# Performance work log

Measured on AMD Instinct MI355X. Metric: run time of the kernel, lower is better.

## Reference

```python
import jax, jax.numpy as jnp
import numpy as np

H = 4
HD = 32
C = 128
NU = 40000
NI = 40000
E = 200000


def _linear(x, W, b):
    # torch Linear: y = x @ W.T + b, W is [out, in]
    return x @ W.T + b


def _counts_in(query, sorted_keys):
    l = jnp.searchsorted(sorted_keys, query, side='left')
    r = jnp.searchsorted(sorted_keys, query, side='right')
    return (r - l).astype(jnp.float32)


def _segment_softmax(scores, seg, n):
    # scores: [E, H], seg: [E] destination ids
    m = jax.ops.segment_max(scores, seg, num_segments=n)
    m = jnp.where(jnp.isfinite(m), m, 0.0)
    e = jnp.exp(scores - m[seg])
    z = jax.ops.segment_sum(e, seg, num_segments=n)
    return e / z[seg]


def _deg_count(idx, n):
    return jnp.zeros((n,), jnp.float32).at[idx].add(1.0)


def _layernorm(x):
    mu = x.mean(-1, keepdims=True)
    var = ((x - mu) ** 2).mean(-1, keepdims=True)
    return (x - mu) / jnp.sqrt(var + 1e-5)


def _relation(x_src, x_dst, src, dst, t_src, t_dst,
              Wq, bq, Wk, bk, Wv, bv, Wo, bo,
              head_bias, beta, tau_raw, gamma, delta,
              counts, recips, n_dst):
    Q = _linear(x_dst, Wq, bq).reshape(-1, H, HD)
    K = _linear(x_src, Wk, bk).reshape(-1, H, HD)
    V = _linear(x_src, Wv, bv).reshape(-1, H, HD)
    Qe, Ke, Ve = Q[dst], K[src], V[src]                      # [E, H, HD]
    scores = (Qe * Ke).sum(-1) / jnp.sqrt(jnp.float32(HD))   # [E, H]
    scores = scores + head_bias
    dt = jnp.abs(t_dst[dst] - t_src[src]) + 1e-6
    tau = jax.nn.softplus(tau_raw) + 1e-6
    scores = scores + (-jnp.log1p(dt / tau))[:, None] * beta
    scores = scores + jnp.log1p(counts)[:, None] * gamma
    scores = scores + recips[:, None] * delta
    w = _segment_softmax(scores, dst, n_dst)                 # [E, H]
    out_e = (Ve * w[:, :, None]).reshape(-1, C)
    out_e = _linear(out_e, Wo, bo)
    return jnp.zeros((n_dst, C), x_dst.dtype).at[dst].add(out_e)


def setup_inputs() -> dict:
    key = jax.random.key(0)
    ks = jax.random.split(key, 20)
    inp = {
        'x_user': jax.random.normal(ks[0], (NU, C), jnp.float32),
        'x_item': jax.random.normal(ks[1], (NI, C), jnp.float32),
        't_user': jax.random.uniform(ks[2], (NU,), jnp.float32) * 100.0,
        't_item': jax.random.uniform(ks[3], (NI,), jnp.float32) * 100.0,
        'edge_index_ui': jax.random.randint(ks[4], (2, E), 0, NU, jnp.int32),
        'edge_index_iu': jax.random.randint(ks[5], (2, E), 0, NI, jnp.int32),
        'Wq': jax.random.normal(ks[6], (C, C), jnp.float32) * 0.05,
        'bq': jax.random.normal(ks[7], (C,), jnp.float32) * 0.05,
        'Wk': jax.random.normal(ks[8], (C, C), jnp.float32) * 0.05,
        'bk': jax.random.normal(ks[9], (C,), jnp.float32) * 0.05,
        'Wv': jax.random.normal(ks[10], (C, C), jnp.float32) * 0.05,
        'bv': jax.random.normal(ks[11], (C,), jnp.float32) * 0.05,
        'Wo': jax.random.normal(ks[12], (C, C), jnp.float32) * 0.05,
        'bo': jax.random.normal(ks[13], (C,), jnp.float32) * 0.05,
        'rel_head_bias': jax.random.normal(ks[14], (2, H), jnp.float32) * 0.1,
        'time_beta': jax.random.normal(ks[15], (2, H), jnp.float32) * 0.1,
        'time_tau_raw': jax.random.normal(ks[16], (2,), jnp.float32),
        'gamma_multirel': jax.random.normal(ks[17], (2, H), jnp.float32) * 0.1,
        'delta_recip': jax.random.normal(ks[18], (2, H), jnp.float32) * 0.1,
    }
    return inp


def reference(x_user, x_item, t_user, t_item, edge_index_ui, edge_index_iu,
              Wq, bq, Wk, bk, Wv, bv, Wo, bo,
              rel_head_bias, time_beta, time_tau_raw, gamma_multirel, delta_recip):
    su, du = edge_index_ui[0], edge_index_ui[1]   # user -> item
    si, di = edge_index_iu[0], edge_index_iu[1]   # item -> user
    # multirel counts (pair multiplicity - 1) and reciprocity flags, per relation
    pid_ui = su * NI + du            # (user,item) pair ids (fits int32: NU*NI < 2^31)
    pid_iu = si * NU + di            # (item,user) pair ids
    rev_for_ui = di * NI + si        # reversed pairs of iu edges in (user,item) space
    rev_for_iu = du * NU + su        # reversed pairs of ui edges in (item,user) space
    counts_ui = _counts_in(pid_ui, jnp.sort(pid_ui)) - 1.0
    counts_iu = _counts_in(pid_iu, jnp.sort(pid_iu)) - 1.0
    recips_ui = (_counts_in(pid_ui, jnp.sort(rev_for_ui)) > 0).astype(jnp.float32)
    recips_iu = (_counts_in(pid_iu, jnp.sort(rev_for_iu)) > 0).astype(jnp.float32)

    out_item = _relation(x_user, x_item, su, du, t_user, t_item,
                         Wq, bq, Wk, bk, Wv, bv, Wo, bo,
                         rel_head_bias[0], time_beta[0], time_tau_raw[0],
                         gamma_multirel[0], delta_recip[0], counts_ui, recips_ui, NI)
    out_user = _relation(x_item, x_user, si, di, t_item, t_user,
                         Wq, bq, Wk, bk, Wv, bv, Wo, bo,
                         rel_head_bias[1], time_beta[1], time_tau_raw[1],
                         gamma_multirel[1], delta_recip[1], counts_iu, recips_iu, NU)
    # degree centrality bias: total (in + out) degree added to every channel
    deg_user = _deg_count(su, NU) + _deg_count(di, NU)
    deg_item = _deg_count(du, NI) + _deg_count(si, NI)
    out_user = out_user + deg_user[:, None]
    out_item = out_item + deg_item[:, None]
    return _layernorm(out_user + x_user), _layernorm(out_item + x_item)
```

## Files before the change

kernel.cpp:

```cpp
#include <hip/hip_runtime.h>
#include <math.h>

constexpr int kH  = 4;
constexpr int kHD = 32;
constexpr int kC  = 128;
constexpr int kNU = 40000;
constexpr int kNI = 40000;
constexpr int kE  = 200000;
constexpr int kNT = kNU + kNI;
constexpr int kTS = 1 << 19;
constexpr int kTMASK = kTS - 1;
constexpr int kSB = (kNT + 1023) / 1024;
constexpr int kTilesPerSide = kNU / 16;
constexpr int kTiles = kNT / 16;
constexpr int kGemmBlocks  = 768;
constexpr int kTableBlocks = 1536;
constexpr int kFusedBlocks = 2304;

#define DEV_INLINE __device__ __forceinline__

typedef short bf16x8 __attribute__((ext_vector_type(8)));
typedef float f32x4  __attribute__((ext_vector_type(4)));
typedef uint32_t u32x4 __attribute__((ext_vector_type(4)));
typedef unsigned long long u64;

DEV_INLINE int hash_slot(int pid) {
  uint32_t h = (uint32_t)pid * 2654435761u;
  return (int)((h >> 13) & kTMASK);
}

DEV_INLINE unsigned short f2bf(float f) {
  uint32_t u = __float_as_uint(f);
  u += 0x7fffu + ((u >> 16) & 1u);
  return (unsigned short)(u >> 16);
}

DEV_INLINE float bflo(uint32_t u) { return __uint_as_float(u << 16); }
DEV_INLINE float bfhi(uint32_t u) { return __uint_as_float(u & 0xffff0000u); }

DEV_INLINE int swz(int row, int elem) {
  return (elem & 7) | (((elem >> 3) ^ (row & 7)) << 3);
}

constexpr u64 kEmpty64 = ~0ULL;

DEV_INLINE void table_insert64(u64* __restrict__ keys, int pid) {
  int slot = hash_slot(pid);
  const u64 want = (u64)(uint32_t)pid | (1ULL << 32);
  for (;;) {
    u64 old = atomicCAS(&keys[slot], kEmpty64, want);
    if (old == kEmpty64) return;
    if ((uint32_t)old == (uint32_t)pid) {
      atomicAdd(&keys[slot], 1ULL << 32);
      return;
    }
    slot = (slot + 1) & kTMASK;
  }
}

DEV_INLINE int table_count64(const u64* __restrict__ keys, int pid) {
  int slot = hash_slot(pid);
  for (;;) {
    u64 k = keys[slot];
    if ((uint32_t)k == (uint32_t)pid) return (int)(k >> 32);
    if (k == kEmpty64) return 0;
    slot = (slot + 1) & kTMASK;
  }
}

__global__ void cast4w_bf16(const float* __restrict__ w0, const float* __restrict__ w1,
                            const float* __restrict__ w2, const float* __restrict__ w3,
                            unsigned short* __restrict__ o0, unsigned short* __restrict__ o1,
                            unsigned short* __restrict__ o2, unsigned short* __restrict__ o3) {
  int i = blockIdx.x * blockDim.x + threadIdx.x;
  int m = i >> 12, j = i & 4095;
  const float* in = (m == 0) ? w0 : (m == 1) ? w1 : (m == 2) ? w2 : w3;
  unsigned short* out = (m == 0) ? o0 : (m == 1) ? o1 : (m == 2) ? o2 : o3;
  float4 v = ((const float4*)in)[j];
  ushort4 o = {f2bf(v.x), f2bf(v.y), f2bf(v.z), f2bf(v.w)};
  ((ushort4*)out)[j] = o;
}

__global__ __launch_bounds__(256, 3) void qkv_build(
    const float* __restrict__ Xu, const float* __restrict__ Xi,
    const unsigned short* __restrict__ Wq, const unsigned short* __restrict__ Wk,
    const unsigned short* __restrict__ Wv,
    const float* __restrict__ bq, const float* __restrict__ bk,
    const float* __restrict__ bv,
    unsigned short* __restrict__ Qu, unsigned short* __restrict__ Ku,
    unsigned short* __restrict__ Vu,
    unsigned short* __restrict__ Qi, unsigned short* __restrict__ Ki,
    unsigned short* __restrict__ Vi,
    const int* __restrict__ su, const int* __restrict__ du,
    const int* __restrict__ si, const int* __restrict__ di,
    u64* __restrict__ keyA, u64* __restrict__ keyB,
    int* __restrict__ deg_all, int* __restrict__ pos_all) {
  __shared__ unsigned short sx[16 * kC];
  __shared__ unsigned short sr[3 * 16 * kC];
  const int bid = blockIdx.x;
  const int tid = threadIdx.x;

  if (bid % 3 != 1) {
    const int tb = (bid / 3) * 2 + ((bid % 3) ? 1 : 0);
    for (int t = tb * 256 + tid; t < 2 * kE; t += kTableBlocks * 256) {
      if (t < kE) {
        int s = su[t], d = du[t];
        table_insert64(keyA, s * kNI + d);
        pos_all[t] = atomicAdd(&deg_all[d], 1);
      } else {
        int e = t - kE;
        int s = si[e], d = di[e];
        table_insert64(keyB, s * kNU + d);
        pos_all[t] = atomicAdd(&deg_all[kNI + d], 1);
      }
    }
    return;
  }

  const int gb   = bid / 3;
  const int wave = tid >> 6;
  const int lane = tid & 63;
  const int mr   = lane & 15;
  const int quad = lane >> 4;
  const int ct0  = wave * 2;
  const int srow = tid >> 4;
  const int schk = tid & 15;

  bf16x8 wf[3][2][4];
  {
    const unsigned short* Ws[3] = {Wq, Wk, Wv};
#pragma unroll
    for (int m = 0; m < 3; ++m)
#pragma unroll
      for (int c = 0; c < 2; ++c) {
        const unsigned short* wrow = Ws[m] + (size_t)((ct0 + c) * 16 + mr) * kC + quad * 8;
#pragma unroll
        for (int kc = 0; kc < 4; ++kc) wf[m][c][kc] = *(const bf16x8*)(wrow + kc * 32);
      }
  }

  int tile = gb;
  float4 xa, xb;
  {
    const bool item = tile >= kTilesPerSide;
    const float* X = item ? Xi : Xu;
    const int base = (item ? tile - kTilesPerSide : tile) * 16;
    const float* xr = X + (size_t)(base + srow) * kC + schk * 8;
    xa = ((const float4*)xr)[0];
    xb = ((const float4*)xr)[1];
  }

  for (; tile < kTiles; tile += kGemmBlocks) {
    const bool item = tile >= kTilesPerSide;
    const int base = (item ? tile - kTilesPerSide : tile) * 16;

    {
      bf16x8 p;
      p[0] = (short)f2bf(xa.x); p[1] = (short)f2bf(xa.y);
      p[2] = (short)f2bf(xa.z); p[3] = (short)f2bf(xa.w);
      p[4] = (short)f2bf(xb.x); p[5] = (short)f2bf(xb.y);
      p[6] = (short)f2bf(xb.z); p[7] = (short)f2bf(xb.w);
      *(bf16x8*)(sx + srow * kC + ((schk ^ (srow & 7)) << 3)) = p;
    }
    __syncthreads();

    bf16x8 b[4];
#pragma unroll
    for (int kc = 0; kc < 4; ++kc)
      b[kc] = *(const bf16x8*)(sx + mr * kC + (((quad + kc * 4) ^ (mr & 7)) << 3));

    int ntile = tile + kGemmBlocks;
    if (ntile < kTiles) {
      const bool nit = ntile >= kTilesPerSide;
      const float* X = nit ? Xi : Xu;
      const int nbase = (nit ? ntile - kTilesPerSide : ntile) * 16;
      const float* xr = X + (size_t)(nbase + srow) * kC + schk * 8;
      xa = ((const float4*)xr)[0];
      xb = ((const float4*)xr)[1];
    }

    f32x4 acc[3][2];
#pragma unroll
    for (int m = 0; m < 3; ++m) {
      acc[m][0] = (f32x4){0.f, 0.f, 0.f, 0.f};
      acc[m][1] = (f32x4){0.f, 0.f, 0.f, 0.f};
    }
#pragma unroll
    for (int kc = 0; kc < 4; ++kc)
#pragma unroll
      for (int m = 0; m < 3; ++m)
#pragma unroll
        for (int c = 0; c < 2; ++c)
          acc[m][c] = __builtin_amdgcn_mfma_f32_16x16x32_bf16(wf[m][c][kc], b[kc], acc[m][c], 0, 0, 0);

    const float* bs[3] = {bq, bk, bv};
#pragma unroll
    for (int m = 0; m < 3; ++m)
#pragma unroll
      for (int c = 0; c < 2; ++c) {
        int c0 = (ct0 + c) * 16 + quad * 4;
        float4 bb = *(const float4*)(bs[m] + c0);
        uint2 p;
        p.x = (uint32_t)f2bf(acc[m][c][0] + bb.x) | ((uint32_t)f2bf(acc[m][c][1] + bb.y) << 16);
        p.y = (uint32_t)f2bf(acc[m][c][2] + bb.z) | ((uint32_t)f2bf(acc[m][c][3] + bb.w) << 16);
        *(uint2*)(sr + (m * 16 + mr) * kC + swz(mr, c0)) = p;
      }
    __syncthreads();

    {
      unsigned short* Os[3] = {item ? Qi : Qu, item ? Ki : Ku, item ? Vi : Vu};
      const int el = (schk ^ (srow & 7)) << 3;
#pragma unroll
      for (int m = 0; m < 3; ++m) {
        bf16x8 v = *(const bf16x8*)(sr + (m * 16 + srow) * kC + el);
        *(bf16x8*)(Os[m] + (size_t)(base + srow) * kC + schk * 8) = v;
      }
    }
  }
}

__global__ __launch_bounds__(256) void scan1(const int* __restrict__ in,
                                             int* __restrict__ out,
                                             int* __restrict__ bsum, int n) {
  __shared__ int sh[256];
  const int t = threadIdx.x;
  const int base = blockIdx.x * 1024 + t * 4;
  int4 v = {0, 0, 0, 0};
  if (base + 3 < n) {
    v = *(const int4*)(in + base);
  } else {
    if (base + 0 < n) v.x = in[base + 0];
    if (base + 1 < n) v.y = in[base + 1];
    if (base + 2 < n) v.z = in[base + 2];
    if (base + 3 < n) v.w = in[base + 3];
  }
  int s = v.x + v.y + v.z + v.w;
  sh[t] = s;
  __syncthreads();
  int val = s;
  for (int off = 1; off < 256; off <<= 1) {
    int add = (t >= off) ? sh[t - off] : 0;
    __syncthreads();
    val += add;
    sh[t] = val;
    __syncthreads();
  }
  int excl = val - s;
  if (base + 0 < n) out[base + 0] = excl;
  if (base + 1 < n) out[base + 1] = excl + v.x;
  if (base + 2 < n) out[base + 2] = excl + v.x + v.y;
  if (base + 3 < n) out[base + 3] = excl + v.x + v.y + v.z;
  if (t == 255) bsum[blockIdx.x] = val;
}

__global__ __launch_bounds__(128) void scan2(const int* __restrict__ bsum,
                                             int* __restrict__ boff,
                                             int* __restrict__ out_total, int nb) {
  __shared__ int sh[128];
  const int t = threadIdx.x;
  int v = (t < nb) ? bsum[t] : 0;
  sh[t] = v;
  __syncthreads();
  int val = v;
  for (int off = 1; off < 128; off <<= 1) {
    int add = (t >= off) ? sh[t - off] : 0;
    __syncthreads();
    val += add;
    sh[t] = val;
    __syncthreads();
  }
  if (t < nb) boff[t] = val - v;
  if (t == nb - 1) *out_total = val;
}

__global__ __launch_bounds__(256) void scan3(int* __restrict__ out,
                                             const int* __restrict__ boff, int n) {
  const int base = blockIdx.x * 1024 + threadIdx.x * 4;
  const int off = boff[blockIdx.x];
#pragma unroll
  for (int i = 0; i < 4; ++i)
    if (base + i < n) out[base + i] += off;
}

__global__ void scatter_bias(const int* __restrict__ su, const int* __restrict__ du,
                             const int* __restrict__ si, const int* __restrict__ di,
                             const float* __restrict__ t_user, const float* __restrict__ t_item,
                             const u64* __restrict__ keyA, const u64* __restrict__ keyB,
                             const int* __restrict__ rp_all, const int* __restrict__ pos_all,
                             int* __restrict__ el_all,
                             const float* __restrict__ hb, const float* __restrict__ beta,
                             const float* __restrict__ taur,
                             const float* __restrict__ gamma, const float* __restrict__ delta,
                             float4* __restrict__ bias_ui, float4* __restrict__ bias_iu) {
  int t = blockIdx.x * blockDim.x + threadIdx.x;
  if (t >= 2 * kE) return;
  const int rel = (t >= kE) ? 1 : 0;
  const int e = rel ? t - kE : t;
  int s, d; float ts, td;
  const u64 *kc_, *kr_;
  int mulC, mulR;
  if (rel == 0) {
    s = su[e]; d = du[e]; ts = t_user[s]; td = t_item[d];
    kc_ = keyA; mulC = kNI;
    kr_ = keyB; mulR = kNU;
  } else {
    s = si[e]; d = di[e]; ts = t_item[s]; td = t_user[d];
    kc_ = keyB; mulC = kNU;
    kr_ = keyA; mulR = kNI;
  }
  const int dg = rel ? kNI + d : d;
  el_all[rp_all[dg] + pos_all[t]] = e;
  float cntv = (float)(table_count64(kc_, s * mulC + d) - 1);
  float rec  = table_count64(kr_, d * mulR + s) > 0 ? 1.0f : 0.0f;
  float dt   = fabsf(td - ts) + 1e-6f;
  float tau  = log1pf(expf(taur[rel])) + 1e-6f;
  float tterm = -log1pf(dt / tau);
  float lc    = log1pf(cntv);
  const float* hp = hb + rel * kH;
  const float* bp = beta + rel * kH;
  const float* gp = gamma + rel * kH;
  const float* dp = delta + rel * kH;
  const float kL2E = 1.4426950408889634f;
  float4 b;
  b.x = (hp[0] + bp[0] * tterm + gp[0] * lc + dp[0] * rec) * kL2E;
  b.y = (hp[1] + bp[1] * tterm + gp[1] * lc + dp[1] * rec) * kL2E;
  b.z = (hp[2] + bp[2] * tterm + gp[2] * lc + dp[2] * rec) * kL2E;
  b.w = (hp[3] + bp[3] * tterm + gp[3] * lc + dp[3] * rec) * kL2E;
  (rel ? bias_iu : bias_ui)[e] = b;
}

__global__ __launch_bounds__(256) void attn_agg(
    const int* __restrict__ rp_all, const int* __restrict__ el_all,
    const int* __restrict__ su, const int* __restrict__ si,
    const unsigned short* __restrict__ Qi, const unsigned short* __restrict__ Ku,
    const unsigned short* __restrict__ Vu,
    const unsigned short* __restrict__ Qu, const unsigned short* __restrict__ Ki,
    const unsigned short* __restrict__ Vi,
    const float* __restrict__ bias_ui, const float* __restrict__ bias_iu,
    unsigned short* __restrict__ h_ui, unsigned short* __restrict__ h_iu) {
  const int wave = threadIdx.x >> 6;
  const int lane = threadIdx.x & 63;
  const int grp  = lane >> 4;
  const int sub  = lane & 15;
  const int h    = sub >> 2;
  const int ch0  = h * kHD + (sub & 3) * 8;
  const int g = blockIdx.x * 4 + wave;
  if (g >= kNT) return;
  const bool isU = g >= kNI;
  const int n = isU ? g - kNI : g;
  const int* rp = rp_all + (isU ? kNI : 0);
  const int* srcA = isU ? si : su;
  const unsigned short* Q = isU ? Qu : Qi;
  const unsigned short* K = isU ? Ki : Ku;
  const unsigned short* V = isU ? Vi : Vu;
  const float* bias = isU ? bias_iu : bias_ui;
  unsigned short* out = isU ? h_iu : h_ui;

  const int beg = rp[n], end = rp[n + 1];
  const float kScaleL2E = 1.4426950408889634f * 0.17677669529663687f;

  float qf[8];
  {
    u32x4 qv = *(const u32x4*)(Q + (size_t)n * kC + ch0);
#pragma unroll
    for (int w = 0; w < 4; ++w) { qf[2 * w] = bflo(qv[w]); qf[2 * w + 1] = bfhi(qv[w]); }
  }

  float z = 0.f;
  float acc[8] = {0.f, 0.f, 0.f, 0.f, 0.f, 0.f, 0.f, 0.f};

  const int p0 = beg + grp;
  int eA = 0, sA = 0;
  if (p0 < end) { eA = el_all[p0]; sA = srcA[eA]; }
  int eB = 0, sB = 0;
  if (p0 + 4 < end) { eB = el_all[p0 + 4]; sB = srcA[eB]; }
  u32x4 kA = *(const u32x4*)(K + (size_t)sA * kC + ch0);
  u32x4 vA = *(const u32x4*)(V + (size_t)sA * kC + ch0);
  float bA = bias[eA * 4 + h];

  for (int p = p0; p < end; p += 4) {
    u32x4 kB = *(const u32x4*)(K + (size_t)sB * kC + ch0);
    u32x4 vB = *(const u32x4*)(V + (size_t)sB * kC + ch0);
    float bB = bias[eB * 4 + h];
    int eC = 0, sC = 0;
    if (p + 8 < end) { eC = el_all[p + 8]; sC = srcA[eC]; }

    float d0 = qf[0] * bflo(kA[0]);
    float d1 = qf[1] * bfhi(kA[0]);
    d0 = fmaf(qf[2], bflo(kA[1]), d0);
    d1 = fmaf(qf[3], bfhi(kA[1]), d1);
    d0 = fmaf(qf[4], bflo(kA[2]), d0);
    d1 = fmaf(qf[5], bfhi(kA[2]), d1);
    d0 = fmaf(qf[6], bflo(kA[3]), d0);
    d1 = fmaf(qf[7], bfhi(kA[3]), d1);
    float dsc = d0 + d1;
    dsc += __shfl_xor(dsc, 1);
    dsc += __shfl_xor(dsc, 2);
    float wgt = __builtin_amdgcn_exp2f(fmaf(dsc, kScaleL2E, bA));
    z += wgt;
#pragma unroll
    for (int w = 0; w < 4; ++w) {
      acc[2 * w]     = fmaf(bflo(vA[w]), wgt, acc[2 * w]);
      acc[2 * w + 1] = fmaf(bfhi(vA[w]), wgt, acc[2 * w + 1]);
    }
    kA = kB; vA = vB; bA = bB; eB = eC; sB = sC;
  }

#pragma unroll
  for (int j = 0; j < 8; ++j) {
    acc[j] += __shfl_xor(acc[j], 16);
    acc[j] += __shfl_xor(acc[j], 32);
  }
  z += __shfl_xor(z, 16);
  z += __shfl_xor(z, 32);

  const float zi = (end > beg) ? 1.0f / z : 0.0f;
  if (grp == 0) {
    bf16x8 o;
#pragma unroll
    for (int j = 0; j < 8; ++j) o[j] = (short)f2bf(acc[j] * zi);
    *(bf16x8*)(out + (size_t)n * kC + ch0) = o;
  }
}

__global__ __launch_bounds__(256, 4) void wo_ln(
    const unsigned short* __restrict__ Hiu, const unsigned short* __restrict__ Hui,
    const unsigned short* __restrict__ Wo,
    const float* __restrict__ Xu, const float* __restrict__ Xi,
    const int* __restrict__ degU, const int* __restrict__ degI,
    const float* __restrict__ bo, float* __restrict__ out) {
  __shared__ unsigned short sh_h[16 * kC];
  __shared__ float sh_p[64 * 2];
  const int tid  = threadIdx.x;
  const int wave = tid >> 6;
  const int lane = tid & 63;
  const int mr   = lane & 15;
  const int quad = lane >> 4;
  const int ct0  = wave * 2;
  const int srow = tid >> 4;
  const int schk = tid & 15;

  bf16x8 wf[2][4];
#pragma unroll
  for (int c = 0; c < 2; ++c) {
    const unsigned short* wrow = Wo + (size_t)((ct0 + c) * 16 + mr) * kC + quad * 8;
#pragma unroll
    for (int kc = 0; kc < 4; ++kc) wf[c][kc] = *(const bf16x8*)(wrow + kc * 32);
  }
  float4 bb[2];
  bb[0] = *(const float4*)(bo + ct0 * 16 + quad * 4);
  bb[1] = *(const float4*)(bo + (ct0 + 1) * 16 + quad * 4);

  int tile = blockIdx.x;
  bf16x8 hv;
  {
    const bool item = tile >= kTilesPerSide;
    const unsigned short* Hs = item ? Hui : Hiu;
    const int base = (item ? tile - kTilesPerSide : tile) * 16;
    hv = *(const bf16x8*)(Hs + (size_t)(base + srow) * kC + schk * 8);
  }

  for (; tile < kTiles; tile += gridDim.x) {
    const bool item = tile >= kTilesPerSide;
    const int base = (item ? tile - kTilesPerSide : tile) * 16;

    *(bf16x8*)(sh_h + srow * kC + ((schk ^ (srow & 7)) << 3)) = hv;
    __syncthreads();

    bf16x8 b[4];
#pragma unroll
    for (int kc = 0; kc < 4; ++kc)
      b[kc] = *(const bf16x8*)(sh_h + mr * kC + (((quad + kc * 4) ^ (mr & 7)) << 3));

    int ntile = tile + gridDim.x;
    if (ntile < kTiles) {
      const bool nit = ntile >= kTilesPerSide;
      const unsigned short* Hs = nit ? Hui : Hiu;
      const int nbase = (nit ? ntile - kTilesPerSide : ntile) * 16;
      hv = *(const bf16x8*)(Hs + (size_t)(nbase + srow) * kC + schk * 8);
    }

    f32x4 acc[2];
    acc[0] = (f32x4){0.f, 0.f, 0.f, 0.f};
    acc[1] = (f32x4){0.f, 0.f, 0.f, 0.f};
#pragma unroll
    for (int kc = 0; kc < 4; ++kc) {
      acc[0] = __builtin_amdgcn_mfma_f32_16x16x32_bf16(wf[0][kc], b[kc], acc[0], 0, 0, 0);
      acc[1] = __builtin_amdgcn_mfma_f32_16x16x32_bf16(wf[1][kc], b[kc], acc[1], 0, 0, 0);
    }

    const int n = base + mr;
    const float* Xs = item ? Xi : Xu;
    const float fdg = (float)(item ? degI[n] : degU[n]);
    float y[8], s1 = 0.f, s2 = 0.f;
#pragma unroll
    for (int c = 0; c < 2; ++c) {
      int c0 = (ct0 + c) * 16 + quad * 4;
      float4 xv = *(const float4*)(Xs + (size_t)n * kC + c0);
      y[c * 4 + 0] = acc[c][0] + xv.x + fdg * bb[c].x;
      y[c * 4 + 1] = acc[c][1] + xv.y + fdg * bb[c].y;
      y[c * 4 + 2] = acc[c][2] + xv.z + fdg * bb[c].z;
      y[c * 4 + 3] = acc[c][3] + xv.w + fdg * bb[c].w;
#pragma unroll
      for (int j = 0; j < 4; ++j) {
        s1 += y[c * 4 + j];
        s2 += y[c * 4 + j] * y[c * 4 + j];
      }
    }
    s1 += __shfl_xor(s1, 16); s2 += __shfl_xor(s2, 16);
    s1 += __shfl_xor(s1, 32); s2 += __shfl_xor(s2, 32);
    if (quad == 0) {
      sh_p[(wave * 16 + mr) * 2]     = s1;
      sh_p[(wave * 16 + mr) * 2 + 1] = s2;
    }
    __syncthreads();
    float t1 = 0.f, t2 = 0.f;
#pragma unroll
    for (int ww = 0; ww < 4; ++ww) {
      t1 += sh_p[(ww * 16 + mr) * 2];
      t2 += sh_p[(ww * 16 + mr) * 2 + 1];
    }
    float mu   = t1 * (1.0f / 128.0f);
    float var  = t2 * (1.0f / 128.0f) - mu * mu;
    float rstd = rsqrtf(fmaxf(var, 0.0f) + 1e-5f);
    float* op = out + (item ? (size_t)kNU * kC : (size_t)0) + (size_t)n * kC;
#pragma unroll
    for (int c = 0; c < 2; ++c) {
      int c0 = (ct0 + c) * 16 + quad * 4;
      float4 o = {(y[c * 4 + 0] - mu) * rstd, (y[c * 4 + 1] - mu) * rstd,
                  (y[c * 4 + 2] - mu) * rstd, (y[c * 4 + 3] - mu) * rstd};
      *(float4*)(op + c0) = o;
    }
  }
}

extern "C" void kernel_launch(void* const* d_in, const int* in_sizes, int n_in,
                              void* d_out, int out_size, void* d_ws, size_t ws_size,
                              hipStream_t stream) {
  const float* x_user = (const float*)d_in[0];
  const float* x_item = (const float*)d_in[1];
  const float* t_user = (const float*)d_in[2];
  const float* t_item = (const float*)d_in[3];
  const int*   eui    = (const int*)d_in[4];
  const int*   eiu    = (const int*)d_in[5];
  const float* Wq = (const float*)d_in[6];
  const float* bq = (const float*)d_in[7];
  const float* Wk = (const float*)d_in[8];
  const float* bk = (const float*)d_in[9];
  const float* Wv = (const float*)d_in[10];
  const float* bv = (const float*)d_in[11];
  const float* Wo = (const float*)d_in[12];
  const float* bo = (const float*)d_in[13];
  const float* hb    = (const float*)d_in[14];
  const float* beta  = (const float*)d_in[15];
  const float* taur  = (const float*)d_in[16];
  const float* gamma = (const float*)d_in[17];
  const float* delta = (const float*)d_in[18];

  const int* su = eui;       const int* du = eui + kE;
  const int* si = eiu;       const int* di = eiu + kE;

  float* w = (float*)d_ws;
  size_t o = 0;
  unsigned short* qu_b = (unsigned short*)(w + o); o += (size_t)kNU * kC / 2;
  unsigned short* ku_b = (unsigned short*)(w + o); o += (size_t)kNU * kC / 2;
  unsigned short* vu_b = (unsigned short*)(w + o); o += (size_t)kNU * kC / 2;
  unsigned short* qi_b = (unsigned short*)(w + o); o += (size_t)kNI * kC / 2;
  unsigned short* ki_b = (unsigned short*)(w + o); o += (size_t)kNI * kC / 2;
  unsigned short* vi_b = (unsigned short*)(w + o); o += (size_t)kNI * kC / 2;
  unsigned short* h_ui = (unsigned short*)(w + o); o += (size_t)kNI * kC / 2;
  unsigned short* h_iu = (unsigned short*)(w + o); o += (size_t)kNU * kC / 2;
  unsigned short* wq_b = (unsigned short*)(w + o); o += kC * kC / 2;
  unsigned short* wk_b = (unsigned short*)(w + o); o += kC * kC / 2;
  unsigned short* wv_b = (unsigned short*)(w + o); o += kC * kC / 2;
  unsigned short* wo_b = (unsigned short*)(w + o); o += kC * kC / 2;
  float* zero_base = w + o;
  int* deg_all = (int*)(w + o); o += kNT;
  size_t zero_bytes = (size_t)((w + o) - zero_base) * sizeof(float);
  o = (o + 1) & ~(size_t)1;
  u64* keyA = (u64*)(w + o); o += (size_t)kTS * 2;
  u64* keyB = (u64*)(w + o); o += (size_t)kTS * 2;
  size_t key_bytes = (size_t)2 * kTS * sizeof(u64);
  float* bias_ui = w + o; o += (size_t)kE * kH;
  float* bias_iu = w + o; o += (size_t)kE * kH;
  int* rp_all  = (int*)(w + o); o += kNT + 1;
  int* el_all  = (int*)(w + o); o += 2 * kE;
  int* bsum    = (int*)(w + o); o += kSB;
  int* boff    = (int*)(w + o); o += kSB;
  int* pos_all = (int*)h_ui;

  hipMemsetAsync(zero_base, 0, zero_bytes, stream);
  hipMemsetAsync(keyA, 0xFF, key_bytes, stream);

  dim3 b256(256);
  cast4w_bf16<<<(4 * kC * kC / 4) / 256, b256, 0, stream>>>(Wq, Wk, Wv, Wo,
                                                            wq_b, wk_b, wv_b, wo_b);

  qkv_build<<<kFusedBlocks, b256, 0, stream>>>(
      x_user, x_item, wq_b, wk_b, wv_b, bq, bk, bv,
      qu_b, ku_b, vu_b, qi_b, ki_b, vi_b,
      su, du, si, di, keyA, keyB, deg_all, pos_all);

  scan1<<<kSB, b256, 0, stream>>>(deg_all, rp_all, bsum, kNT);
  scan2<<<1, dim3(128), 0, stream>>>(bsum, boff, rp_all + kNT, kSB);
  scan3<<<kSB, b256, 0, stream>>>(rp_all, boff, kNT);

  int g2E = (2 * kE + 255) / 256;
  scatter_bias<<<g2E, b256, 0, stream>>>(su, du, si, di, t_user, t_item,
                                         keyA, keyB, rp_all, pos_all, el_all,
                                         hb, beta, taur, gamma, delta,
                                         (float4*)bias_ui, (float4*)bias_iu);

  attn_agg<<<kNT / 4, b256, 0, stream>>>(rp_all, el_all, su, si,
                                         qi_b, ku_b, vu_b, qu_b, ki_b, vi_b,
                                         bias_ui, bias_iu, h_ui, h_iu);

  wo_ln<<<768, b256, 0, stream>>>(h_iu, h_ui, wo_b, x_user, x_item,
                                  deg_all + kNI, deg_all, bo, (float*)d_out);
}
```

Before: 264.0 us.

## Replace hash-table pair counting with CSR neighbor scans and packed edge lists

Drops the two open-addressing hash tables, along with their 0xFF memset and atomic CAS inserts, that counted multi-edges and detected reciprocal edges. Those counts are now found by scanning the short per-destination CSR lists, which store each edge id packed with its source id. The final scan3 pass is removed by adding the block offset on each row-pointer read, and attn_agg reads the source id from the packed entry instead of doing a dependent gather. In exchange there is one extra kernel launch, a wider 64-bit edge list, and per-edge linear scans whose cost grows with node degree.

After: 254.5 us. -3.6%, faster.

```diff
diff --git a/kernel.cpp b/kernel.cpp
--- a/kernel.cpp
+++ b/kernel.cpp
@@ -8,8 +8,6 @@
 constexpr int kNI = 40000;
 constexpr int kE  = 200000;
 constexpr int kNT = kNU + kNI;
-constexpr int kTS = 1 << 19;
-constexpr int kTMASK = kTS - 1;
 constexpr int kSB = (kNT + 1023) / 1024;
 constexpr int kTilesPerSide = kNU / 16;
 constexpr int kTiles = kNT / 16;
@@ -24,11 +22,6 @@
 typedef uint32_t u32x4 __attribute__((ext_vector_type(4)));
 typedef unsigned long long u64;
 
-DEV_INLINE int hash_slot(int pid) {
-  uint32_t h = (uint32_t)pid * 2654435761u;
-  return (int)((h >> 13) & kTMASK);
-}
-
 DEV_INLINE unsigned short f2bf(float f) {
   uint32_t u = __float_as_uint(f);
   u += 0x7fffu + ((u >> 16) & 1u);
@@ -42,30 +35,8 @@
   return (elem & 7) | (((elem >> 3) ^ (row & 7)) << 3);
 }
 
-constexpr u64 kEmpty64 = ~0ULL;
-
-DEV_INLINE void table_insert64(u64* __restrict__ keys, int pid) {
-  int slot = hash_slot(pid);
-  const u64 want = (u64)(uint32_t)pid | (1ULL << 32);
-  for (;;) {
-    u64 old = atomicCAS(&keys[slot], kEmpty64, want);
-    if (old == kEmpty64) return;
-    if ((uint32_t)old == (uint32_t)pid) {
-      atomicAdd(&keys[slot], 1ULL << 32);
-      return;
-    }
-    slot = (slot + 1) & kTMASK;
-  }
-}
-
-DEV_INLINE int table_count64(const u64* __restrict__ keys, int pid) {
-  int slot = hash_slot(pid);
-  for (;;) {
-    u64 k = keys[slot];
-    if ((uint32_t)k == (uint32_t)pid) return (int)(k >> 32);
-    if (k == kEmpty64) return 0;
-    slot = (slot + 1) & kTMASK;
-  }
+DEV_INLINE int rpf(const int* __restrict__ rp, const int* __restrict__ boff, int i) {
+  return rp[i] + boff[i >> 10];
 }
 
 __global__ void cast4w_bf16(const float* __restrict__ w0, const float* __restrict__ w1,
@@ -91,9 +62,7 @@
     unsigned short* __restrict__ Vu,
     unsigned short* __restrict__ Qi, unsigned short* __restrict__ Ki,
     unsigned short* __restrict__ Vi,
-    const int* __restrict__ su, const int* __restrict__ du,
-    const int* __restrict__ si, const int* __restrict__ di,
-    u64* __restrict__ keyA, u64* __restrict__ keyB,
+    const int* __restrict__ du, const int* __restrict__ di,
     int* __restrict__ deg_all, int* __restrict__ pos_all) {
   __shared__ unsigned short sx[16 * kC];
   __shared__ unsigned short sr[3 * 16 * kC];
@@ -104,14 +73,9 @@
     const int tb = (bid / 3) * 2 + ((bid % 3) ? 1 : 0);
     for (int t = tb * 256 + tid; t < 2 * kE; t += kTableBlocks * 256) {
       if (t < kE) {
-        int s = su[t], d = du[t];
-        table_insert64(keyA, s * kNI + d);
-        pos_all[t] = atomicAdd(&deg_all[d], 1);
+        pos_all[t] = atomicAdd(&deg_all[du[t]], 1);
       } else {
-        int e = t - kE;
-        int s = si[e], d = di[e];
-        table_insert64(keyB, s * kNU + d);
-        pos_all[t] = atomicAdd(&deg_all[kNI + d], 1);
+        pos_all[t] = atomicAdd(&deg_all[kNI + di[t - kE]], 1);
       }
     }
     return;
@@ -255,7 +219,7 @@
 
 __global__ __launch_bounds__(128) void scan2(const int* __restrict__ bsum,
                                              int* __restrict__ boff,
-                                             int* __restrict__ out_total, int nb) {
+                                             int* __restrict__ rp_tail, int nb) {
   __shared__ int sh[128];
   const int t = threadIdx.x;
   int v = (t < nb) ? bsum[t] : 0;
@@ -270,48 +234,54 @@
     __syncthreads();
   }
   if (t < nb) boff[t] = val - v;
-  if (t == nb - 1) *out_total = val;
-}
-
-__global__ __launch_bounds__(256) void scan3(int* __restrict__ out,
-                                             const int* __restrict__ boff, int n) {
-  const int base = blockIdx.x * 1024 + threadIdx.x * 4;
-  const int off = boff[blockIdx.x];
-#pragma unroll
-  for (int i = 0; i < 4; ++i)
-    if (base + i < n) out[base + i] += off;
-}
-
-__global__ void scatter_bias(const int* __restrict__ su, const int* __restrict__ du,
-                             const int* __restrict__ si, const int* __restrict__ di,
-                             const float* __restrict__ t_user, const float* __restrict__ t_item,
-                             const u64* __restrict__ keyA, const u64* __restrict__ keyB,
-                             const int* __restrict__ rp_all, const int* __restrict__ pos_all,
-                             int* __restrict__ el_all,
-                             const float* __restrict__ hb, const float* __restrict__ beta,
-                             const float* __restrict__ taur,
-                             const float* __restrict__ gamma, const float* __restrict__ delta,
-                             float4* __restrict__ bias_ui, float4* __restrict__ bias_iu) {
+  if (t == nb - 1) *rp_tail = v;
+}
+
+__global__ void scatter_pk(const int* __restrict__ su, const int* __restrict__ du,
+                           const int* __restrict__ si, const int* __restrict__ di,
+                           const int* __restrict__ rp_all, const int* __restrict__ boff,
+                           const int* __restrict__ pos_all,
+                           u64* __restrict__ el_all) {
+  int t = blockIdx.x * blockDim.x + threadIdx.x;
+  if (t >= 2 * kE) return;
+  int e, s, dg;
+  if (t < kE) { e = t;       s = su[e]; dg = du[e]; }
+  else        { e = t - kE;  s = si[e]; dg = kNI + di[e]; }
+  el_all[rpf(rp_all, boff, dg) + pos_all[t]] = (u64)(uint32_t)e | ((u64)(uint32_t)s << 32);
+}
+
+__global__ void bias_csr(const int* __restrict__ su, const int* __restrict__ du,
+                         const int* __restrict__ si, const int* __restrict__ di,
+                         const float* __restrict__ t_user, const float* __restrict__ t_item,
+                         const int* __restrict__ rp_all, const int* __restrict__ boff,
+                         const u64* __restrict__ el_all,
+                         const float* __restrict__ hb, const float* __restrict__ beta,
+                         const float* __restrict__ taur,
+                         const float* __restrict__ gamma, const float* __restrict__ delta,
+                         float4* __restrict__ bias_ui, float4* __restrict__ bias_iu) {
   int t = blockIdx.x * blockDim.x + threadIdx.x;
   if (t >= 2 * kE) return;
   const int rel = (t >= kE) ? 1 : 0;
   const int e = rel ? t - kE : t;
-  int s, d; float ts, td;
-  const u64 *kc_, *kr_;
-  int mulC, mulR;
+  int s, d; float ts, td; int dg, rg;
   if (rel == 0) {
     s = su[e]; d = du[e]; ts = t_user[s]; td = t_item[d];
-    kc_ = keyA; mulC = kNI;
-    kr_ = keyB; mulR = kNU;
+    dg = d;
+    rg = kNI + s;
   } else {
     s = si[e]; d = di[e]; ts = t_item[s]; td = t_user[d];
-    kc_ = keyB; mulC = kNU;
-    kr_ = keyA; mulR = kNI;
-  }
-  const int dg = rel ? kNI + d : d;
-  el_all[rp_all[dg] + pos_all[t]] = e;
-  float cntv = (float)(table_count64(kc_, s * mulC + d) - 1);
-  float rec  = table_count64(kr_, d * mulR + s) > 0 ? 1.0f : 0.0f;
+    dg = kNI + d;
+    rg = s;
+  }
+  int b0 = rpf(rp_all, boff, dg), b1 = rpf(rp_all, boff, dg + 1);
+  int cnt = 0;
+  for (int p = b0; p < b1; ++p) cnt += ((int)(el_all[p] >> 32) == s);
+  int r0 = rpf(rp_all, boff, rg), r1 = rpf(rp_all, boff, rg + 1);
+  int rcp = 0;
+  for (int p = r0; p < r1; ++p) rcp |= ((int)(el_all[p] >> 32) == d);
+
+  float cntv = (float)(cnt - 1);
+  float rec  = (float)rcp;
   float dt   = fabsf(td - ts) + 1e-6f;
   float tau  = log1pf(expf(taur[rel])) + 1e-6f;
   float tterm = -log1pf(dt / tau);
@@ -330,8 +300,8 @@
 }
 
 __global__ __launch_bounds__(256) void attn_agg(
-    const int* __restrict__ rp_all, const int* __restrict__ el_all,
-    const int* __restrict__ su, const int* __restrict__ si,
+    const int* __restrict__ rp_all, const int* __restrict__ boff,
+    const u64* __restrict__ el_all,
     const unsigned short* __restrict__ Qi, const unsigned short* __restrict__ Ku,
     const unsigned short* __restrict__ Vu,
     const unsigned short* __restrict__ Qu, const unsigned short* __restrict__ Ki,
@@ -348,15 +318,13 @@
   if (g >= kNT) return;
   const bool isU = g >= kNI;
   const int n = isU ? g - kNI : g;
-  const int* rp = rp_all + (isU ? kNI : 0);
-  const int* srcA = isU ? si : su;
   const unsigned short* Q = isU ? Qu : Qi;
   const unsigned short* K = isU ? Ki : Ku;
   const unsigned short* V = isU ? Vi : Vu;
   const float* bias = isU ? bias_iu : bias_ui;
   unsigned short* out = isU ? h_iu : h_ui;
 
-  const int beg = rp[n], end = rp[n + 1];
+  const int beg = rpf(rp_all, boff, g), end = rpf(rp_all, boff, g + 1);
   const float kScaleL2E = 1.4426950408889634f * 0.17677669529663687f;
 
   float qf[8];
@@ -371,9 +339,9 @@
 
   const int p0 = beg + grp;
   int eA = 0, sA = 0;
-  if (p0 < end) { eA = el_all[p0]; sA = srcA[eA]; }
+  if (p0 < end) { u64 pk = el_all[p0]; eA = (int)pk; sA = (int)(pk >> 32); }
   int eB = 0, sB = 0;
-  if (p0 + 4 < end) { eB = el_all[p0 + 4]; sB = srcA[eB]; }
+  if (p0 + 4 < end) { u64 pk = el_all[p0 + 4]; eB = (int)pk; sB = (int)(pk >> 32); }
   u32x4 kA = *(const u32x4*)(K + (size_t)sA * kC + ch0);
   u32x4 vA = *(const u32x4*)(V + (size_t)sA * kC + ch0);
   float bA = bias[eA * 4 + h];
@@ -383,7 +351,7 @@
     u32x4 vB = *(const u32x4*)(V + (size_t)sB * kC + ch0);
     float bB = bias[eB * 4 + h];
     int eC = 0, sC = 0;
-    if (p + 8 < end) { eC = el_all[p + 8]; sC = srcA[eC]; }
+    if (p + 8 < end) { u64 pk = el_all[p + 8]; eC = (int)pk; sC = (int)(pk >> 32); }
 
     float d0 = qf[0] * bflo(kA[0]);
     float d1 = qf[1] * bfhi(kA[0]);
@@ -577,20 +545,16 @@
   float* zero_base = w + o;
   int* deg_all = (int*)(w + o); o += kNT;
   size_t zero_bytes = (size_t)((w + o) - zero_base) * sizeof(float);
-  o = (o + 1) & ~(size_t)1;
-  u64* keyA = (u64*)(w + o); o += (size_t)kTS * 2;
-  u64* keyB = (u64*)(w + o); o += (size_t)kTS * 2;
-  size_t key_bytes = (size_t)2 * kTS * sizeof(u64);
   float* bias_ui = w + o; o += (size_t)kE * kH;
   float* bias_iu = w + o; o += (size_t)kE * kH;
   int* rp_all  = (int*)(w + o); o += kNT + 1;
-  int* el_all  = (int*)(w + o); o += 2 * kE;
   int* bsum    = (int*)(w + o); o += kSB;
   int* boff    = (int*)(w + o); o += kSB;
+  o = (o + 1) & ~(size_t)1;
+  u64* el_all  = (u64*)(w + o); o += (size_t)2 * kE * 2;
   int* pos_all = (int*)h_ui;
 
   hipMemsetAsync(zero_base, 0, zero_bytes, stream);
-  hipMemsetAsync(keyA, 0xFF, key_bytes, stream);
 
   dim3 b256(256);
   cast4w_bf16<<<(4 * kC * kC / 4) / 256, b256, 0, stream>>>(Wq, Wk, Wv, Wo,
@@ -599,19 +563,20 @@
   qkv_build<<<kFusedBlocks, b256, 0, stream>>>(
       x_user, x_item, wq_b, wk_b, wv_b, bq, bk, bv,
       qu_b, ku_b, vu_b, qi_b, ki_b, vi_b,
-      su, du, si, di, keyA, keyB, deg_all, pos_all);
+      du, di, deg_all, pos_all);
 
   scan1<<<kSB, b256, 0, stream>>>(deg_all, rp_all, bsum, kNT);
   scan2<<<1, dim3(128), 0, stream>>>(bsum, boff, rp_all + kNT, kSB);
-  scan3<<<kSB, b256, 0, stream>>>(rp_all, boff, kNT);
 
   int g2E = (2 * kE + 255) / 256;
-  scatter_bias<<<g2E, b256, 0, stream>>>(su, du, si, di, t_user, t_item,
-                                         keyA, keyB, rp_all, pos_all, el_all,
-                                         hb, beta, taur, gamma, delta,
-                                         (float4*)bias_ui, (float4*)bias_iu);
-
-  attn_agg<<<kNT / 4, b256, 0, stream>>>(rp_all, el_all, su, si,
+  scatter_pk<<<g2E, b256, 0, stream>>>(su, du, si, di, rp_all, boff, pos_all, el_all);
+
+  bias_csr<<<g2E, b256, 0, stream>>>(su, du, si, di, t_user, t_item,
+                                     rp_all, boff, el_all,
+                                     hb, beta, taur, gamma, delta,
+                                     (float4*)bias_ui, (float4*)bias_iu);
+
+  attn_agg<<<kNT / 4, b256, 0, stream>>>(rp_all, boff, el_all,
                                          qi_b, ku_b, vu_b, qu_b, ki_b, vi_b,
                                          bias_ui, bias_iu, h_ui, h_iu);
 
```
